# Optimization experiments

Hardware: AMD Instinct MI355X
Metric: run time of the kernel (lower is better)

Reference implementation:

```python
import jax, jax.numpy as jnp
import numpy as np

N_NODES = 50000
N_EDGES = 400000
N_GRAPHS = 250
D = 256
NUM_FEATURES = 256
NUM_CLASSES = 10
N_EXTRA_LAYERS = 4  # num_layers - 1
BN_EPS = 1e-5


def _mean_agg(x, src, dst, n):
    # DGL copy_u + mean over incoming edges; zero in-degree nodes get 0.
    s = jax.ops.segment_sum(x[src], dst, num_segments=n)           # [N, d]
    deg = jax.ops.segment_sum(jnp.ones((src.shape[0],), x.dtype), dst, num_segments=n)
    deg = deg[:, None]
    return jnp.where(deg > 0, s / jnp.maximum(deg, 1.0), 0.0)


def _gin_layer(x, src, dst, W1, b1, W2, b2, gamma, beta):
    n = x.shape[0]
    h = x + _mean_agg(x, src, dst, n)                              # (1+eps)*x + agg, eps=0
    h = jax.nn.relu(h @ W1 + b1) @ W2 + b2                         # apply_func MLP
    h = jax.nn.relu(h)                                             # GINConv activation
    mu = h.mean(axis=0)
    var = h.var(axis=0)                                            # biased var (torch BN train)
    return gamma * (h - mu) / jnp.sqrt(var + BN_EPS) + beta


def setup_inputs() -> dict:
    key = jax.random.key(0)
    ks = jax.random.split(key, 24)
    sc_in = 1.0 / np.sqrt(NUM_FEATURES)
    sc = 1.0 / np.sqrt(D)
    inp = {
        "x": jax.random.normal(ks[0], (N_NODES, NUM_FEATURES), dtype=jnp.float32),
        "src": jax.random.randint(ks[1], (N_EDGES,), 0, N_NODES, dtype=jnp.int32),
        "dst": jax.random.randint(ks[2], (N_EDGES,), 0, N_NODES, dtype=jnp.int32),
        "node_counts": jnp.full((N_GRAPHS,), N_NODES // N_GRAPHS, dtype=jnp.int32),
        # conv1 MLP + BN1
        "W1a": jax.random.normal(ks[3], (NUM_FEATURES, D), dtype=jnp.float32) * sc_in,
        "b1a": jnp.zeros((D,), jnp.float32),
        "W1b": jax.random.normal(ks[4], (D, D), dtype=jnp.float32) * sc,
        "b1b": jnp.zeros((D,), jnp.float32),
        "g1": jnp.ones((D,), jnp.float32),
        "be1": jnp.zeros((D,), jnp.float32),
        # stacked convs 2..5 + BNs
        "Ws1": jax.random.normal(ks[5], (N_EXTRA_LAYERS, D, D), dtype=jnp.float32) * sc,
        "bs1": jnp.zeros((N_EXTRA_LAYERS, D), jnp.float32),
        "Ws2": jax.random.normal(ks[6], (N_EXTRA_LAYERS, D, D), dtype=jnp.float32) * sc,
        "bs2": jnp.zeros((N_EXTRA_LAYERS, D), jnp.float32),
        "gammas": jnp.ones((N_EXTRA_LAYERS, D), jnp.float32),
        "betas": jnp.zeros((N_EXTRA_LAYERS, D), jnp.float32),
        # classifier
        "fcW1": jax.random.normal(ks[7], (D, D), dtype=jnp.float32) * sc,
        "fcb1": jnp.zeros((D,), jnp.float32),
        "fcW2": jax.random.normal(ks[8], (D, NUM_CLASSES), dtype=jnp.float32) * sc,
        "fcb2": jnp.zeros((NUM_CLASSES,), jnp.float32),
    }
    return inp


def reference(x, src, dst, node_counts, W1a, b1a, W1b, b1b, g1, be1,
              Ws1, bs1, Ws2, bs2, gammas, betas, fcW1, fcb1, fcW2, fcb2):
    h = _gin_layer(x, src, dst, W1a, b1a, W1b, b1b, g1, be1)
    for i in range(N_EXTRA_LAYERS):
        h = _gin_layer(h, src, dst, Ws1[i], bs1[i], Ws2[i], bs2[i], gammas[i], betas[i])
    # per-graph last-node readout
    last_idx = jnp.cumsum(node_counts) - 1                          # [n_graphs]
    g = h[last_idx]                                                 # [n_graphs, d]
    # dropout is identity in eval mode
    g = jax.nn.relu(g @ fcW1 + fcb1)
    logits = g @ fcW2 + fcb2
    return jax.nn.log_softmax(logits, axis=-1)
```

## Files before the change

### kernel.cpp

```cpp
#include <hip/hip_runtime.h>
#include <hip/hip_bf16.h>

#define N_NODESC 50000
#define N_EDGESC 400000
#define N_GRAPHSC 250
#define DDIM 256
#define NCLS 10
#define BN_EPSF 1e-5f
#define MPAD 50048
#define NBLK_SCAN 196

typedef __attribute__((ext_vector_type(4))) float f32x4;
typedef __attribute__((ext_vector_type(8))) short bf16x8;
typedef __attribute__((ext_vector_type(8))) unsigned short u16x8;

__device__ __forceinline__ float bf2f(unsigned short h) {
    union { unsigned int u; float f; } c;
    c.u = ((unsigned int)h) << 16;
    return c.f;
}
__device__ __forceinline__ unsigned short f2bf(float f) {
    union { float f; unsigned int u; } c;
    c.f = f;
    unsigned int u = c.u;
    return (unsigned short)((u + 0x7FFFu + ((u >> 16) & 1u)) >> 16);
}

__device__ __forceinline__ void gld_lds16(const void* g, void* l) {
    __builtin_amdgcn_global_load_lds(
        (const __attribute__((address_space(1))) unsigned int*)g,
        (__attribute__((address_space(3))) unsigned int*)l, 16, 0, 0);
}


__global__ void k_zero32(int* __restrict__ p, int n) {
    int i = blockIdx.x * blockDim.x + threadIdx.x;
    if (i < n) p[i] = 0;
}

__global__ void k_count(const int* __restrict__ dst, int* __restrict__ cnt) {
    int e = blockIdx.x * blockDim.x + threadIdx.x;
    if (e < N_EDGESC) atomicAdd(&cnt[dst[e]], 1);
}

__global__ __launch_bounds__(256) void k_scan1(const int* __restrict__ deg,
                                               int* __restrict__ rowstart,
                                               int* __restrict__ bsum) {
    __shared__ int sh[256];
    int tid = threadIdx.x;
    int i = blockIdx.x * 256 + tid;
    int v = (i < N_NODESC) ? deg[i] : 0;
    sh[tid] = v;
    __syncthreads();
    for (int off = 1; off < 256; off <<= 1) {
        int t = (tid >= off) ? sh[tid - off] : 0;
        __syncthreads();
        sh[tid] += t;
        __syncthreads();
    }
    if (i < N_NODESC) rowstart[i] = sh[tid] - v;
    if (tid == 255) bsum[blockIdx.x] = sh[255];
}

__global__ __launch_bounds__(256) void k_scan2(int* __restrict__ rowstart,
                                               const int* __restrict__ bsum) {
    __shared__ int sh[256];
    int tid = threadIdx.x;
    sh[tid] = (tid < NBLK_SCAN) ? bsum[tid] : 0;
    __syncthreads();
    for (int off = 1; off < 256; off <<= 1) {
        int t = (tid >= off) ? sh[tid - off] : 0;
        __syncthreads();
        sh[tid] += t;
        __syncthreads();
    }
    int i = blockIdx.x * 256 + tid;
    if (blockIdx.x > 0 && i < N_NODESC) rowstart[i] += sh[blockIdx.x - 1];
    if (i == 0) rowstart[N_NODESC] = N_EDGESC;
}

__global__ void k_fill(const int* __restrict__ src, const int* __restrict__ dst,
                       const int* __restrict__ rowstart, int* __restrict__ cur,
                       int* __restrict__ esrc) {
    int e = blockIdx.x * blockDim.x + threadIdx.x;
    if (e < N_EDGESC) {
        int d = dst[e];
        int pos = rowstart[d] + atomicAdd(&cur[d], 1);
        esrc[pos] = src[e];
    }
}


__global__ __launch_bounds__(256) void k_wprep(const float* __restrict__ W1a,
                                               const float* __restrict__ W1b,
                                               const float* __restrict__ Ws1,
                                               const float* __restrict__ Ws2,
                                               unsigned short* __restrict__ Wt) {
    int i = blockIdx.x * blockDim.x + threadIdx.x;
    if (i >= 10 * 65536) return;
    int m = i >> 16;
    int r = i & 65535;
    int n = r >> 8;
    int k = r & 255;
    int l = m >> 1, wsel = m & 1;
    const float* src = (l == 0) ? (wsel ? W1b : W1a)
                                : (wsel ? Ws2 + (size_t)(l - 1) * 65536
                                        : Ws1 + (size_t)(l - 1) * 65536);
    Wt[i] = f2bf(src[(size_t)k * 256 + n]);
}

__global__ __launch_bounds__(256) void k_xbf(const float* __restrict__ X,
                                             unsigned short* __restrict__ Y) {
    int i = blockIdx.x * 256 + threadIdx.x;
    if (i < N_NODESC * 64) {
        float4 v = ((const float4*)X)[i];
        ushort4 o;
        o.x = f2bf(v.x); o.y = f2bf(v.y); o.z = f2bf(v.z); o.w = f2bf(v.w);
        ((ushort4*)Y)[i] = o;
    }
}

__global__ void k_zeropad(unsigned short* __restrict__ b1) {
    int i = blockIdx.x * blockDim.x + threadIdx.x;
    int npad = (MPAD - N_NODESC) * DDIM;
    if (i < npad) b1[(size_t)N_NODESC * DDIM + i] = 0;
}

__global__ __launch_bounds__(256) void k_agg_bf(const unsigned short* __restrict__ X,
                                                const int* __restrict__ esrc,
                                                const int* __restrict__ rowstart,
                                                const float* __restrict__ stat,
                                                const float* __restrict__ gamma,
                                                const float* __restrict__ beta,
                                                unsigned short* __restrict__ Hout) {
    int node = blockIdx.x * 4 + (threadIdx.x >> 6);
    if (node >= N_NODESC) return;
    int lane = threadIdx.x & 63;
    int d0 = lane * 4;
    float sc[4], tt[4];
    if (stat) {
        const float invN = 1.0f / (float)N_NODESC;
#pragma unroll
        for (int q = 0; q < 4; q++) {
            float mu = stat[d0 + q] * invN;
            float var = stat[256 + d0 + q] * invN - mu * mu;
            float s = gamma[d0 + q] * rsqrtf(var + BN_EPSF);
            sc[q] = s;
            tt[q] = beta[d0 + q] - s * mu;
        }
    } else {
#pragma unroll
        for (int q = 0; q < 4; q++) { sc[q] = 1.f; tt[q] = 0.f; }
    }
    int beg = rowstart[node];
    int end = rowstart[node + 1];
    float a0 = 0.f, a1 = 0.f, a2 = 0.f, a3 = 0.f;
    float b0 = 0.f, b1 = 0.f, b2 = 0.f, b3 = 0.f;
    int j = beg;
    for (; j + 2 <= end; j += 2) {
        int sn0 = esrc[j];
        int sn1 = esrc[j + 1];
        ushort4 v0 = *(const ushort4*)(X + (size_t)sn0 * DDIM + d0);
        ushort4 v1 = *(const ushort4*)(X + (size_t)sn1 * DDIM + d0);
        a0 += bf2f(v0.x); a1 += bf2f(v0.y); a2 += bf2f(v0.z); a3 += bf2f(v0.w);
        b0 += bf2f(v1.x); b1 += bf2f(v1.y); b2 += bf2f(v1.z); b3 += bf2f(v1.w);
    }
    if (j < end) {
        int sn0 = esrc[j];
        ushort4 v0 = *(const ushort4*)(X + (size_t)sn0 * DDIM + d0);
        a0 += bf2f(v0.x); a1 += bf2f(v0.y); a2 += bf2f(v0.z); a3 += bf2f(v0.w);
    }
    a0 += b0; a1 += b1; a2 += b2; a3 += b3;
    float inv = (end > beg) ? 1.0f / (float)(end - beg) : 0.0f;
    float cnt = (end > beg) ? 2.0f : 1.0f;
    ushort4 xv = *(const ushort4*)(X + (size_t)node * DDIM + d0);
    ushort4 o;
    o.x = f2bf(sc[0] * (bf2f(xv.x) + a0 * inv) + tt[0] * cnt);
    o.y = f2bf(sc[1] * (bf2f(xv.y) + a1 * inv) + tt[1] * cnt);
    o.z = f2bf(sc[2] * (bf2f(xv.z) + a2 * inv) + tt[2] * cnt);
    o.w = f2bf(sc[3] * (bf2f(xv.w) + a3 * inv) + tt[3] * cnt);
    *(ushort4*)(Hout + (size_t)node * DDIM + d0) = o;
}


__global__ __launch_bounds__(256) void k_mlp(const unsigned short* __restrict__ A,
                                             const unsigned short* __restrict__ W1t,
                                             const float* __restrict__ b1,
                                             const unsigned short* __restrict__ W2t,
                                             const float* __restrict__ b2,
                                             unsigned short* __restrict__ C,
                                             float* __restrict__ stat) {
    __shared__ unsigned short Tl[128 * 256];
    __shared__ unsigned short As[128 * 32];
    __shared__ unsigned short Bs[128 * 32];

    const int tid = threadIdx.x;
    const int wv = tid >> 6;
    const int lane = tid & 63;
    const int bm = blockIdx.x;
    const int wr = (wv >> 1) * 64;
    const int wc = (wv & 1) * 64;
    const int lr = lane & 15;
    const int lk = lane >> 4;

    for (int nh = 0; nh < 2; nh++) {
        f32x4 acc[4][4];
#pragma unroll
        for (int m = 0; m < 4; m++)
#pragma unroll
            for (int n = 0; n < 4; n++) acc[m][n] = (f32x4)(0.f);

        for (int k0 = 0; k0 < 256; k0 += 32) {
#pragma unroll
            for (int i = 0; i < 2; i++) {
                int c = wv * 128 + i * 64 + lane;
                int row = c >> 2;
                int kc = (c & 3) ^ ((row >> 1) & 3);
                gld_lds16(A + (size_t)(bm * 128 + row) * 256 + k0 + kc * 8,
                          (void*)&As[(size_t)(wv * 128 + i * 64) * 8]);
                gld_lds16(W1t + (size_t)(nh * 128 + row) * 256 + k0 + kc * 8,
                          (void*)&Bs[(size_t)(wv * 128 + i * 64) * 8]);
            }
            __syncthreads();
            bf16x8 af[4], bfr[4];
#pragma unroll
            for (int m = 0; m < 4; m++) {
                int row = wr + m * 16 + lr;
                af[m] = ((const bf16x8*)As)[row * 4 + (lk ^ ((row >> 1) & 3))];
            }
#pragma unroll
            for (int n = 0; n < 4; n++) {
                int row = wc + n * 16 + lr;
                bfr[n] = ((const bf16x8*)Bs)[row * 4 + (lk ^ ((row >> 1) & 3))];
            }
#pragma unroll
            for (int m = 0; m < 4; m++)
#pragma unroll
                for (int n = 0; n < 4; n++)
                    acc[m][n] = __builtin_amdgcn_mfma_f32_16x16x32_bf16(
                        af[m], bfr[n], acc[m][n], 0, 0, 0);
            __syncthreads();
        }
#pragma unroll
        for (int n = 0; n < 4; n++) {
            int col = nh * 128 + wc + n * 16 + lr;
            float bv = b1[col];
#pragma unroll
            for (int m = 0; m < 4; m++)
#pragma unroll
                for (int i = 0; i < 4; i++) {
                    int row = wr + m * 16 + lk * 4 + i;
                    float v = fmaxf(acc[m][n][i] + bv, 0.f);
                    int cs = (col >> 3) ^ (row & 7);
                    Tl[row * 256 + cs * 8 + (col & 7)] = f2bf(v);
                }
        }
    }
    __syncthreads();

    for (int nh = 0; nh < 2; nh++) {
        f32x4 acc[4][4];
#pragma unroll
        for (int m = 0; m < 4; m++)
#pragma unroll
            for (int n = 0; n < 4; n++) acc[m][n] = (f32x4)(0.f);

        for (int k0 = 0; k0 < 256; k0 += 32) {
#pragma unroll
            for (int i = 0; i < 2; i++) {
                int c = wv * 128 + i * 64 + lane;
                int row = c >> 2;
                int kc = (c & 3) ^ ((row >> 1) & 3);
                gld_lds16(W2t + (size_t)(nh * 128 + row) * 256 + k0 + kc * 8,
                          (void*)&Bs[(size_t)(wv * 128 + i * 64) * 8]);
            }
            __syncthreads();
            bf16x8 af[4], bfr[4];
#pragma unroll
            for (int m = 0; m < 4; m++) {
                int row = wr + m * 16 + lr;
                int cs = ((k0 >> 3) + lk) ^ (row & 7);
                af[m] = ((const bf16x8*)Tl)[row * 32 + cs];
            }
#pragma unroll
            for (int n = 0; n < 4; n++) {
                int row = wc + n * 16 + lr;
                bfr[n] = ((const bf16x8*)Bs)[row * 4 + (lk ^ ((row >> 1) & 3))];
            }
#pragma unroll
            for (int m = 0; m < 4; m++)
#pragma unroll
                for (int n = 0; n < 4; n++)
                    acc[m][n] = __builtin_amdgcn_mfma_f32_16x16x32_bf16(
                        af[m], bfr[n], acc[m][n], 0, 0, 0);
            __syncthreads();
        }
#pragma unroll
        for (int n = 0; n < 4; n++) {
            int col = nh * 128 + wc + n * 16 + lr;
            float bv = b2[col];
            float sp = 0.f, ssp = 0.f;
#pragma unroll
            for (int m = 0; m < 4; m++)
#pragma unroll
                for (int i = 0; i < 4; i++) {
                    int row = bm * 128 + wr + m * 16 + lk * 4 + i;
                    float v = fmaxf(acc[m][n][i] + bv, 0.f);
                    C[(size_t)row * 256 + col] = f2bf(v);
                    if (row < N_NODESC) { sp += v; ssp += v * v; }
                }
            sp += __shfl_xor(sp, 16);
            sp += __shfl_xor(sp, 32);
            ssp += __shfl_xor(ssp, 16);
            ssp += __shfl_xor(ssp, 32);
            if (lane < 16) {
                atomicAdd(&stat[col], sp);
                atomicAdd(&stat[256 + col], ssp);
            }
        }
    }
}


__global__ __launch_bounds__(256) void k_head(const unsigned short* __restrict__ Y,
                                              const int* __restrict__ counts,
                                              const float* __restrict__ stat,
                                              const float* __restrict__ gamma,
                                              const float* __restrict__ beta,
                                              const float* __restrict__ fcW1,
                                              const float* __restrict__ fcb1,
                                              const float* __restrict__ fcW2,
                                              const float* __restrict__ fcb2,
                                              float* __restrict__ out) {
    int g = blockIdx.x;
    __shared__ float row[DDIM];
    __shared__ float gv[DDIM];
    __shared__ float logits[NCLS];
    __shared__ int lastIdx;
    if (threadIdx.x == 0) {
        int s = 0;
        for (int i = 0; i <= g; i++) s += counts[i];
        lastIdx = s - 1;
    }
    __syncthreads();
    int j = threadIdx.x;
    const float invN = 1.0f / (float)N_NODESC;
    float mu = stat[j] * invN;
    float var = stat[256 + j] * invN - mu * mu;
    float sc = gamma[j] * rsqrtf(var + BN_EPSF);
    row[j] = sc * (bf2f(Y[(size_t)lastIdx * DDIM + j]) - mu) + beta[j];
    __syncthreads();
    float acc = fcb1[j];
    for (int d = 0; d < DDIM; d++) acc += row[d] * fcW1[(size_t)d * DDIM + j];
    gv[j] = fmaxf(acc, 0.f);
    __syncthreads();
    if (j < NCLS) {
        float a = fcb2[j];
        for (int d = 0; d < DDIM; d++) a += gv[d] * fcW2[(size_t)d * NCLS + j];
        logits[j] = a;
    }
    __syncthreads();
    if (j == 0) {
        float m = -1e30f;
        for (int c = 0; c < NCLS; c++) m = fmaxf(m, logits[c]);
        float se = 0.f;
        for (int c = 0; c < NCLS; c++) se += expf(logits[c] - m);
        float lse = m + logf(se);
        for (int c = 0; c < NCLS; c++) out[g * NCLS + c] = logits[c] - lse;
    }
}


extern "C" void kernel_launch(void* const* d_in, const int* in_sizes, int n_in,
                              void* d_out, int out_size, void* d_ws, size_t ws_size,
                              hipStream_t stream) {
    const float* x    = (const float*)d_in[0];
    const int* src    = (const int*)d_in[1];
    const int* dst    = (const int*)d_in[2];
    const int* counts = (const int*)d_in[3];
    const float* W1a  = (const float*)d_in[4];
    const float* b1a  = (const float*)d_in[5];
    const float* W1b  = (const float*)d_in[6];
    const float* b1b  = (const float*)d_in[7];
    const float* g1   = (const float*)d_in[8];
    const float* be1  = (const float*)d_in[9];
    const float* Ws1  = (const float*)d_in[10];
    const float* bs1  = (const float*)d_in[11];
    const float* Ws2  = (const float*)d_in[12];
    const float* bs2  = (const float*)d_in[13];
    const float* gms  = (const float*)d_in[14];
    const float* bts  = (const float*)d_in[15];
    const float* fcW1 = (const float*)d_in[16];
    const float* fcb1 = (const float*)d_in[17];
    const float* fcW2 = (const float*)d_in[18];
    const float* fcb2 = (const float*)d_in[19];
    float* out = (float*)d_out;

    char* ws = (char*)d_ws;
    const size_t BUF = (size_t)MPAD * DDIM * 2;
    unsigned short* B0 = (unsigned short*)(ws);
    unsigned short* B1 = (unsigned short*)(ws + BUF);
    unsigned short* Bx = (unsigned short*)(ws + 2 * BUF);
    unsigned short* Wt = (unsigned short*)(ws + 3 * BUF);
    int* rowstart      = (int*)(ws + 3 * BUF + 1310720);
    int* cursor        = (int*)(ws + 3 * BUF + 1510784);
    int* esrc          = (int*)(ws + 3 * BUF + 1710848);
    float* colsum      = (float*)(ws + 3 * BUF + 3310848);
    int* bsum          = (int*)(ws + 3 * BUF + 3312896);

    k_zero32<<<dim3((N_NODESC + 255) / 256), 256, 0, stream>>>(cursor, N_NODESC);
    k_count<<<dim3((N_EDGESC + 255) / 256), 256, 0, stream>>>(dst, cursor);
    k_scan1<<<dim3(NBLK_SCAN), 256, 0, stream>>>(cursor, rowstart, bsum);
    k_scan2<<<dim3(NBLK_SCAN), 256, 0, stream>>>(rowstart, bsum);
    k_zero32<<<dim3((N_NODESC + 255) / 256), 256, 0, stream>>>(cursor, N_NODESC);
    k_fill<<<dim3((N_EDGESC + 255) / 256), 256, 0, stream>>>(src, dst, rowstart,
                                                             cursor, esrc);

    k_wprep<<<dim3((10 * 65536 + 255) / 256), 256, 0, stream>>>(W1a, W1b, Ws1, Ws2, Wt);
    k_xbf<<<dim3(12500), 256, 0, stream>>>(x, Bx);
    k_zeropad<<<dim3(((MPAD - N_NODESC) * DDIM + 255) / 256), 256, 0, stream>>>(B1);

    for (int l = 0; l < 5; ++l) {
        const float* B1b = (l == 0) ? b1a : bs1 + (l - 1) * 256;
        const float* B2b = (l == 0) ? b1b : bs2 + (l - 1) * 256;
        const unsigned short* Wt1 = Wt + (size_t)(l * 2) * 65536;
        const unsigned short* Wt2 = Wt + (size_t)(l * 2 + 1) * 65536;

        if (l == 0) {
            k_agg_bf<<<dim3(12500), 256, 0, stream>>>(Bx, esrc, rowstart, nullptr,
                                                      nullptr, nullptr, B1);
        } else {
            const float* GA = (l == 1) ? g1 : gms + (l - 2) * 256;
            const float* BE = (l == 1) ? be1 : bts + (l - 2) * 256;
            k_agg_bf<<<dim3(12500), 256, 0, stream>>>(B0, esrc, rowstart, colsum,
                                                      GA, BE, B1);
        }
        k_zero32<<<1, 512, 0, stream>>>((int*)colsum, 512);
        k_mlp<<<dim3(MPAD / 128), 256, 0, stream>>>(B1, Wt1, B1b, Wt2, B2b, B0,
                                                    colsum);
    }

    k_head<<<dim3(N_GRAPHSC), 256, 0, stream>>>(B0, counts, colsum,
                                                gms + 3 * 256, bts + 3 * 256,
                                                fcW1, fcb1, fcW2, fcb2, out);
}
```

Baseline: 572.6 us.

## Use 512-thread MLP blocks loading operands directly from global, unroll aggregation by four

The fused two-layer MLP kernel now runs 8 waves per 128-row block, each wave covering a 64x64 tile of the full 256-wide output, so the split into two column halves goes away. The LDS staging buffers for A and W, along with their per-step barriers, are removed, and MFMA operands are read straight from global memory through the cache. The edge-aggregation loop is unrolled from two to four neighbours with independent accumulators so more gathers are in flight. The cost is uncoalesced, repeated global reads of A and the weights that previously went through LDS, plus higher register pressure.

```diff
diff --git a/kernel.cpp b/kernel.cpp
--- a/kernel.cpp
+++ b/kernel.cpp
@@ -24,12 +24,6 @@
     c.f = f;
     unsigned int u = c.u;
     return (unsigned short)((u + 0x7FFFu + ((u >> 16) & 1u)) >> 16);
-}
-
-__device__ __forceinline__ void gld_lds16(const void* g, void* l) {
-    __builtin_amdgcn_global_load_lds(
-        (const __attribute__((address_space(1))) unsigned int*)g,
-        (__attribute__((address_space(3))) unsigned int*)l, 16, 0, 0);
 }
 
 
@@ -156,21 +150,26 @@
     int end = rowstart[node + 1];
     float a0 = 0.f, a1 = 0.f, a2 = 0.f, a3 = 0.f;
     float b0 = 0.f, b1 = 0.f, b2 = 0.f, b3 = 0.f;
+    float c0 = 0.f, c1 = 0.f, c2 = 0.f, c3 = 0.f;
+    float e0 = 0.f, e1 = 0.f, e2 = 0.f, e3 = 0.f;
     int j = beg;
-    for (; j + 2 <= end; j += 2) {
-        int sn0 = esrc[j];
-        int sn1 = esrc[j + 1];
+    for (; j + 4 <= end; j += 4) {
+        int sn0 = esrc[j], sn1 = esrc[j + 1], sn2 = esrc[j + 2], sn3 = esrc[j + 3];
         ushort4 v0 = *(const ushort4*)(X + (size_t)sn0 * DDIM + d0);
         ushort4 v1 = *(const ushort4*)(X + (size_t)sn1 * DDIM + d0);
+        ushort4 v2 = *(const ushort4*)(X + (size_t)sn2 * DDIM + d0);
+        ushort4 v3 = *(const ushort4*)(X + (size_t)sn3 * DDIM + d0);
         a0 += bf2f(v0.x); a1 += bf2f(v0.y); a2 += bf2f(v0.z); a3 += bf2f(v0.w);
         b0 += bf2f(v1.x); b1 += bf2f(v1.y); b2 += bf2f(v1.z); b3 += bf2f(v1.w);
-    }
-    if (j < end) {
+        c0 += bf2f(v2.x); c1 += bf2f(v2.y); c2 += bf2f(v2.z); c3 += bf2f(v2.w);
+        e0 += bf2f(v3.x); e1 += bf2f(v3.y); e2 += bf2f(v3.z); e3 += bf2f(v3.w);
+    }
+    for (; j < end; j++) {
         int sn0 = esrc[j];
         ushort4 v0 = *(const ushort4*)(X + (size_t)sn0 * DDIM + d0);
         a0 += bf2f(v0.x); a1 += bf2f(v0.y); a2 += bf2f(v0.z); a3 += bf2f(v0.w);
     }
-    a0 += b0; a1 += b1; a2 += b2; a3 += b3;
+    a0 += b0 + c0 + e0; a1 += b1 + c1 + e1; a2 += b2 + c2 + e2; a3 += b3 + c3 + e3;
     float inv = (end > beg) ? 1.0f / (float)(end - beg) : 0.0f;
     float cnt = (end > beg) ? 2.0f : 1.0f;
     ushort4 xv = *(const ushort4*)(X + (size_t)node * DDIM + d0);
@@ -183,140 +182,109 @@
 }
 
 
-__global__ __launch_bounds__(256) void k_mlp(const unsigned short* __restrict__ A,
-                                             const unsigned short* __restrict__ W1t,
-                                             const float* __restrict__ b1,
-                                             const unsigned short* __restrict__ W2t,
-                                             const float* __restrict__ b2,
-                                             unsigned short* __restrict__ C,
-                                             float* __restrict__ stat) {
+__global__ __launch_bounds__(512, 4) void k_mlp(const unsigned short* __restrict__ A,
+                                                const unsigned short* __restrict__ W1t,
+                                                const float* __restrict__ b1,
+                                                const unsigned short* __restrict__ W2t,
+                                                const float* __restrict__ b2,
+                                                unsigned short* __restrict__ C,
+                                                float* __restrict__ stat) {
     __shared__ unsigned short Tl[128 * 256];
-    __shared__ unsigned short As[128 * 32];
-    __shared__ unsigned short Bs[128 * 32];
 
     const int tid = threadIdx.x;
     const int wv = tid >> 6;
     const int lane = tid & 63;
     const int bm = blockIdx.x;
-    const int wr = (wv >> 1) * 64;
-    const int wc = (wv & 1) * 64;
+    const int wr = (wv >> 2) * 64;
+    const int wc = (wv & 3) * 64;
     const int lr = lane & 15;
     const int lk = lane >> 4;
 
-    for (int nh = 0; nh < 2; nh++) {
-        f32x4 acc[4][4];
+    f32x4 acc[4][4];
+
+#pragma unroll
+    for (int m = 0; m < 4; m++)
+#pragma unroll
+        for (int n = 0; n < 4; n++) acc[m][n] = (f32x4)(0.f);
+
+    for (int k0 = 0; k0 < 256; k0 += 32) {
+        bf16x8 af[4], bfr[4];
 #pragma unroll
         for (int m = 0; m < 4; m++)
-#pragma unroll
-            for (int n = 0; n < 4; n++) acc[m][n] = (f32x4)(0.f);
-
-        for (int k0 = 0; k0 < 256; k0 += 32) {
-#pragma unroll
-            for (int i = 0; i < 2; i++) {
-                int c = wv * 128 + i * 64 + lane;
-                int row = c >> 2;
-                int kc = (c & 3) ^ ((row >> 1) & 3);
-                gld_lds16(A + (size_t)(bm * 128 + row) * 256 + k0 + kc * 8,
-                          (void*)&As[(size_t)(wv * 128 + i * 64) * 8]);
-                gld_lds16(W1t + (size_t)(nh * 128 + row) * 256 + k0 + kc * 8,
-                          (void*)&Bs[(size_t)(wv * 128 + i * 64) * 8]);
+            af[m] = *(const bf16x8*)(A + (size_t)(bm * 128 + wr + m * 16 + lr) * 256 +
+                                     k0 + lk * 8);
+#pragma unroll
+        for (int n = 0; n < 4; n++)
+            bfr[n] = *(const bf16x8*)(W1t + (size_t)(wc + n * 16 + lr) * 256 +
+                                      k0 + lk * 8);
+#pragma unroll
+        for (int m = 0; m < 4; m++)
+#pragma unroll
+            for (int n = 0; n < 4; n++)
+                acc[m][n] = __builtin_amdgcn_mfma_f32_16x16x32_bf16(af[m], bfr[n],
+                                                                    acc[m][n], 0, 0, 0);
+    }
+#pragma unroll
+    for (int n = 0; n < 4; n++) {
+        int col = wc + n * 16 + lr;
+        float bv = b1[col];
+#pragma unroll
+        for (int m = 0; m < 4; m++)
+#pragma unroll
+            for (int i = 0; i < 4; i++) {
+                int row = wr + m * 16 + lk * 4 + i;
+                float v = fmaxf(acc[m][n][i] + bv, 0.f);
+                int cs = (col >> 3) ^ (row & 7);
+                Tl[row * 256 + cs * 8 + (col & 7)] = f2bf(v);
             }
-            __syncthreads();
-            bf16x8 af[4], bfr[4];
-#pragma unroll
-            for (int m = 0; m < 4; m++) {
-                int row = wr + m * 16 + lr;
-                af[m] = ((const bf16x8*)As)[row * 4 + (lk ^ ((row >> 1) & 3))];
+    }
+    __syncthreads();
+
+#pragma unroll
+    for (int m = 0; m < 4; m++)
+#pragma unroll
+        for (int n = 0; n < 4; n++) acc[m][n] = (f32x4)(0.f);
+
+    for (int k0 = 0; k0 < 256; k0 += 32) {
+        bf16x8 af[4], bfr[4];
+#pragma unroll
+        for (int m = 0; m < 4; m++) {
+            int row = wr + m * 16 + lr;
+            int cs = ((k0 >> 3) + lk) ^ (row & 7);
+            af[m] = ((const bf16x8*)Tl)[row * 32 + cs];
+        }
+#pragma unroll
+        for (int n = 0; n < 4; n++)
+            bfr[n] = *(const bf16x8*)(W2t + (size_t)(wc + n * 16 + lr) * 256 +
+                                      k0 + lk * 8);
+#pragma unroll
+        for (int m = 0; m < 4; m++)
+#pragma unroll
+            for (int n = 0; n < 4; n++)
+                acc[m][n] = __builtin_amdgcn_mfma_f32_16x16x32_bf16(af[m], bfr[n],
+                                                                    acc[m][n], 0, 0, 0);
+    }
+#pragma unroll
+    for (int n = 0; n < 4; n++) {
+        int col = wc + n * 16 + lr;
+        float bv = b2[col];
+        float sp = 0.f, ssp = 0.f;
+#pragma unroll
+        for (int m = 0; m < 4; m++)
+#pragma unroll
+            for (int i = 0; i < 4; i++) {
+                int row = bm * 128 + wr + m * 16 + lk * 4 + i;
+                float v = fmaxf(acc[m][n][i] + bv, 0.f);
+                C[(size_t)row * 256 + col] = f2bf(v);
+                if (row < N_NODESC) { sp += v; ssp += v * v; }
             }
-#pragma unroll
-            for (int n = 0; n < 4; n++) {
-                int row = wc + n * 16 + lr;
-                bfr[n] = ((const bf16x8*)Bs)[row * 4 + (lk ^ ((row >> 1) & 3))];
-            }
-#pragma unroll
-            for (int m = 0; m < 4; m++)
-#pragma unroll
-                for (int n = 0; n < 4; n++)
-                    acc[m][n] = __builtin_amdgcn_mfma_f32_16x16x32_bf16(
-                        af[m], bfr[n], acc[m][n], 0, 0, 0);
-            __syncthreads();
-        }
-#pragma unroll
-        for (int n = 0; n < 4; n++) {
-            int col = nh * 128 + wc + n * 16 + lr;
-            float bv = b1[col];
-#pragma unroll
-            for (int m = 0; m < 4; m++)
-#pragma unroll
-                for (int i = 0; i < 4; i++) {
-                    int row = wr + m * 16 + lk * 4 + i;
-                    float v = fmaxf(acc[m][n][i] + bv, 0.f);
-                    int cs = (col >> 3) ^ (row & 7);
-                    Tl[row * 256 + cs * 8 + (col & 7)] = f2bf(v);
-                }
-        }
-    }
-    __syncthreads();
-
-    for (int nh = 0; nh < 2; nh++) {
-        f32x4 acc[4][4];
-#pragma unroll
-        for (int m = 0; m < 4; m++)
-#pragma unroll
-            for (int n = 0; n < 4; n++) acc[m][n] = (f32x4)(0.f);
-
-        for (int k0 = 0; k0 < 256; k0 += 32) {
-#pragma unroll
-            for (int i = 0; i < 2; i++) {
-                int c = wv * 128 + i * 64 + lane;
-                int row = c >> 2;
-                int kc = (c & 3) ^ ((row >> 1) & 3);
-                gld_lds16(W2t + (size_t)(nh * 128 + row) * 256 + k0 + kc * 8,
-                          (void*)&Bs[(size_t)(wv * 128 + i * 64) * 8]);
-            }
-            __syncthreads();
-            bf16x8 af[4], bfr[4];
-#pragma unroll
-            for (int m = 0; m < 4; m++) {
-                int row = wr + m * 16 + lr;
-                int cs = ((k0 >> 3) + lk) ^ (row & 7);
-                af[m] = ((const bf16x8*)Tl)[row * 32 + cs];
-            }
-#pragma unroll
-            for (int n = 0; n < 4; n++) {
-                int row = wc + n * 16 + lr;
-                bfr[n] = ((const bf16x8*)Bs)[row * 4 + (lk ^ ((row >> 1) & 3))];
-            }
-#pragma unroll
-            for (int m = 0; m < 4; m++)
-#pragma unroll
-                for (int n = 0; n < 4; n++)
-                    acc[m][n] = __builtin_amdgcn_mfma_f32_16x16x32_bf16(
-                        af[m], bfr[n], acc[m][n], 0, 0, 0);
-            __syncthreads();
-        }
-#pragma unroll
-        for (int n = 0; n < 4; n++) {
-            int col = nh * 128 + wc + n * 16 + lr;
-            float bv = b2[col];
-            float sp = 0.f, ssp = 0.f;
-#pragma unroll
-            for (int m = 0; m < 4; m++)
-#pragma unroll
-                for (int i = 0; i < 4; i++) {
-                    int row = bm * 128 + wr + m * 16 + lk * 4 + i;
-                    float v = fmaxf(acc[m][n][i] + bv, 0.f);
-                    C[(size_t)row * 256 + col] = f2bf(v);
-                    if (row < N_NODESC) { sp += v; ssp += v * v; }
-                }
-            sp += __shfl_xor(sp, 16);
-            sp += __shfl_xor(sp, 32);
-            ssp += __shfl_xor(ssp, 16);
-            ssp += __shfl_xor(ssp, 32);
-            if (lane < 16) {
-                atomicAdd(&stat[col], sp);
-                atomicAdd(&stat[256 + col], ssp);
-            }
+        sp += __shfl_xor(sp, 16);
+        sp += __shfl_xor(sp, 32);
+        ssp += __shfl_xor(ssp, 16);
+        ssp += __shfl_xor(ssp, 32);
+        if (lane < 16) {
+            atomicAdd(&stat[col], sp);
+            atomicAdd(&stat[256 + col], ssp);
         }
     }
 }
@@ -436,7 +404,7 @@
                                                       GA, BE, B1);
         }
         k_zero32<<<1, 512, 0, stream>>>((int*)colsum, 512);
-        k_mlp<<<dim3(MPAD / 128), 256, 0, stream>>>(B1, Wt1, B1b, Wt2, B2b, B0,
+        k_mlp<<<dim3(MPAD / 128), 512, 0, stream>>>(B1, Wt1, B1b, Wt2, B2b, B0,
                                                     colsum);
     }
 
```

Result: slower. 587.6 us (+2.6%).
